# Performance work log

Measured on AMD Instinct MI355X. Metric: run time of the kernel, lower is better.

## Reference

```python
import jax, jax.numpy as jnp
import numpy as np

N = 100000      # number of entities
E = 400000      # number of edges (before self-loops)
D = 200         # feature_dim
D0 = 100        # init_fea_dim
NREL = 475      # 2*num_rels + 1 (self-loop relation = NREL-1)
NBR = 100       # num_base_r
B = 1024        # query batch
L = 2           # number of cells / layers
EPS = 1e-5


def _bn(x, g, b):
    # BatchNorm1d, training-mode batch statistics (biased var), per-feature affine
    m = jnp.mean(x, axis=0)
    v = jnp.var(x, axis=0)
    return (x - m) * jax.lax.rsqrt(v + EPS) * g + b


def setup_inputs() -> dict:
    key = jax.random.key(0)
    ks = jax.random.split(key, 12)
    return {
        # graph (edge list form of the DGL graph g)
        "src_id": jax.random.randint(ks[0], (E,), 0, N),
        "dst_id": jax.random.randint(ks[1], (E,), 0, N),
        "e_type": jax.random.randint(ks[2], (E,), 0, NREL - 1),  # NREL-1 reserved for self-loop
        # link-prediction queries
        "subj": jax.random.randint(ks[3], (B,), 0, N),
        "rel": jax.random.randint(ks[4], (B,), 0, NREL),
        # learned parameters
        "emb_h": jax.random.normal(ks[5], (N, D0), dtype=jnp.float32) * 0.02,
        "emb_e": jax.random.normal(ks[6], (NBR, D), dtype=jnp.float32) * 0.1,
        "lin_w": jax.random.normal(ks[7], (D0, D), dtype=jnp.float32) * (1.0 / np.sqrt(D0)),
        "lin_b": jnp.zeros((D,), dtype=jnp.float32),
        "rel_wt": jax.random.normal(ks[8], (NREL, NBR), dtype=jnp.float32) * 0.1,
        "w_rel": jax.random.normal(ks[9], (D, D), dtype=jnp.float32) * (1.0 / np.sqrt(D)),
        # per-cell params, stacked over L layers
        "agg_bn_g": jnp.ones((L, D), dtype=jnp.float32),
        "agg_bn_b": jnp.zeros((L, D), dtype=jnp.float32),
        "cell_bn_g": jnp.ones((L, D), dtype=jnp.float32),
        "cell_bn_b": jnp.zeros((L, D), dtype=jnp.float32),
        "concat_w": jax.random.normal(ks[10], (L, D, D), dtype=jnp.float32) * (1.0 / np.sqrt(D)),
        "concat_b": jnp.zeros((L, D), dtype=jnp.float32),
    }


def reference(src_id, dst_id, e_type, subj, rel,
              emb_h, emb_e, lin_w, lin_b, rel_wt, w_rel,
              agg_bn_g, agg_bn_b, cell_bn_g, cell_bn_b, concat_w, concat_b):
    nodes = jnp.arange(N, dtype=src_id.dtype)
    # append self-loops for every node, with the dedicated self-loop relation id
    src_f = jnp.concatenate([src_id, nodes])                      # [E+N]
    dst_f = jnp.concatenate([dst_id, nodes])                      # [E+N]
    et_f = jnp.concatenate([e_type, jnp.full((N,), NREL - 1, dtype=e_type.dtype)])

    all_ent = emb_h @ lin_w + lin_b                               # [N, D]
    rel_embed = rel_wt @ emb_e                                    # [NREL, D]

    for i in range(L):
        src_emb = all_ent[src_f]                                  # [E+N, D] per-edge gather
        hr = rel_embed[et_f]                                      # [E+N, D] per-edge gather
        zero_out = src_emb * hr                                   # pre_mult op (no BN/ReLU)
        agg = jax.ops.segment_sum(zero_out, dst_f, num_segments=N)  # edge -> node aggregation
        agg = jax.nn.relu(_bn(agg, agg_bn_g[i], agg_bn_b[i]))     # OpModule BN + ReLU
        h = agg @ concat_w[i] + concat_b[i]                       # Cell concat Linear (1 concat node)
        all_ent = jax.nn.relu(_bn(h, cell_bn_g[i], cell_bn_b[i]))  # Cell BN + ReLU
        rel_embed = rel_embed @ w_rel                             # per-layer relation transform

    # DistMult score function: [B, N]
    score = (all_ent[subj] * rel_embed[rel]) @ all_ent.T
    return score
```

## Files before the change

### kernel.cpp

```cpp
#include <hip/hip_runtime.h>


#define N_ENT  100000
#define N_EDGE 400000
#define N_EF   500000
#define D_     200
#define D0_    100
#define NREL_  475
#define B_     1024
#define GSTAT2 2048
#define KP_D   224
#define KP_D0  128

typedef unsigned short ushort_t;
typedef __attribute__((ext_vector_type(8))) short bf16x8;
typedef __attribute__((ext_vector_type(4))) float f32x4;

__device__ __forceinline__ ushort_t f2bf(float x) {
  unsigned u = __float_as_uint(x);
  return (ushort_t)((u + 0x7FFFu + ((u >> 16) & 1u)) >> 16);
}
__device__ __forceinline__ float bf2f(ushort_t h) {
  return __uint_as_float(((unsigned)h) << 16);
}

__device__ __forceinline__ void gld16(const void* g, void* l) {
  __builtin_amdgcn_global_load_lds(
      (const __attribute__((address_space(1))) unsigned*)g,
      (__attribute__((address_space(3))) unsigned*)l, 16, 0, 0);
}


__global__ void k_hist(const int* __restrict__ dst_id, int* __restrict__ cnt) {
  int e = blockIdx.x * 256 + threadIdx.x;
  if (e < N_EF) {
    int d = (e < N_EDGE) ? dst_id[e] : (e - N_EDGE);
    atomicAdd(&cnt[d], 1);
  }
}

__global__ __launch_bounds__(256) void k_scan_block(const int* __restrict__ cnt,
                                                    int* __restrict__ rp,
                                                    int* __restrict__ bsum) {
  __shared__ int sm[256];
  int tid = threadIdx.x;
  int base = blockIdx.x * 1024 + tid * 4;
  int v0 = (base + 0 < N_ENT) ? cnt[base + 0] : 0;
  int v1 = (base + 1 < N_ENT) ? cnt[base + 1] : 0;
  int v2 = (base + 2 < N_ENT) ? cnt[base + 2] : 0;
  int v3 = (base + 3 < N_ENT) ? cnt[base + 3] : 0;
  int tsum = v0 + v1 + v2 + v3;
  sm[tid] = tsum;
  __syncthreads();
  for (int off = 1; off < 256; off <<= 1) {
    int t = (tid >= off) ? sm[tid - off] : 0;
    __syncthreads();
    sm[tid] += t;
    __syncthreads();
  }
  int run = sm[tid] - tsum;
  if (base + 0 < N_ENT) { rp[base + 0] = run; } run += v0;
  if (base + 1 < N_ENT) { rp[base + 1] = run; } run += v1;
  if (base + 2 < N_ENT) { rp[base + 2] = run; } run += v2;
  if (base + 3 < N_ENT) { rp[base + 3] = run; }
  if (tid == 255) bsum[blockIdx.x] = sm[255];
}

__global__ void k_scan_tops(int* __restrict__ bsum, int nb) {
  __shared__ int sm[256];
  int tid = threadIdx.x;
  int v = (tid < nb) ? bsum[tid] : 0;
  sm[tid] = v;
  __syncthreads();
  for (int off = 1; off < 256; off <<= 1) {
    int t = (tid >= off) ? sm[tid - off] : 0;
    __syncthreads();
    sm[tid] += t;
    __syncthreads();
  }
  if (tid < nb) bsum[tid] = sm[tid] - v;
}

__global__ void k_scan_add(int* __restrict__ rp, const int* __restrict__ bsum,
                           int* __restrict__ cursor) {
  int i = blockIdx.x * 256 + threadIdx.x;
  if (i < N_ENT) {
    int r = rp[i] + bsum[i >> 10];
    rp[i] = r;
    cursor[i] = r;
  }
}

__global__ void k_fill(const int* __restrict__ src_id, const int* __restrict__ dst_id,
                       const int* __restrict__ e_type, int* __restrict__ cursor,
                       int* __restrict__ cs, int* __restrict__ ct) {
  int e = blockIdx.x * 256 + threadIdx.x;
  if (e < N_EF) {
    int s, d, t;
    if (e < N_EDGE) { s = src_id[e]; d = dst_id[e]; t = e_type[e]; }
    else            { s = e - N_EDGE; d = s; t = NREL_ - 1; }
    int pos = atomicAdd(&cursor[d], 1);
    cs[pos] = s;
    ct[pos] = t;
  }
}


template <bool BN>
__global__ __launch_bounds__(256) void k_aggregate(const float* __restrict__ ent,
                                                   const float* __restrict__ relE,
                                                   const int* __restrict__ rp,
                                                   const int* __restrict__ cnt,
                                                   const int* __restrict__ cs,
                                                   const int* __restrict__ ct,
                                                   float* __restrict__ out,
                                                   const float* __restrict__ scale,
                                                   const float* __restrict__ shift) {
  int n = blockIdx.x;
  int f = threadIdx.x;
  if (f >= D_) return;
  float sc = 0.f, sh = 0.f;
  if (BN) { sc = scale[f]; sh = shift[f]; }
  int s0 = rp[n], e0 = s0 + cnt[n];
  float a0 = 0.f, a1 = 0.f, a2 = 0.f, a3 = 0.f;
  int idx = s0;
  for (; idx + 4 <= e0; idx += 4) {
    int sA = cs[idx + 0], tA = ct[idx + 0];
    int sB = cs[idx + 1], tB = ct[idx + 1];
    int sC = cs[idx + 2], tC = ct[idx + 2];
    int sD = cs[idx + 3], tD = ct[idx + 3];
    float eA = ent[(long)sA * D_ + f], rA = relE[(long)tA * D_ + f];
    float eB = ent[(long)sB * D_ + f], rB = relE[(long)tB * D_ + f];
    float eC = ent[(long)sC * D_ + f], rC = relE[(long)tC * D_ + f];
    float eD = ent[(long)sD * D_ + f], rD = relE[(long)tD * D_ + f];
    if (BN) {
      eA = fmaxf(fmaf(eA, sc, sh), 0.f);
      eB = fmaxf(fmaf(eB, sc, sh), 0.f);
      eC = fmaxf(fmaf(eC, sc, sh), 0.f);
      eD = fmaxf(fmaf(eD, sc, sh), 0.f);
    }
    a0 = fmaf(eA, rA, a0);
    a1 = fmaf(eB, rB, a1);
    a2 = fmaf(eC, rC, a2);
    a3 = fmaf(eD, rD, a3);
  }
  for (; idx < e0; ++idx) {
    int sA = cs[idx], tA = ct[idx];
    float eA = ent[(long)sA * D_ + f];
    if (BN) eA = fmaxf(fmaf(eA, sc, sh), 0.f);
    a0 = fmaf(eA, relE[(long)tA * D_ + f], a0);
  }
  out[(long)n * D_ + f] = (a0 + a1) + (a2 + a3);
}

__global__ __launch_bounds__(64) void k_colstats(const float* __restrict__ X,
                                                 double* __restrict__ part) {
  int t = threadIdx.x;
  if (t >= 50) return;
  double s0 = 0, s1 = 0, s2 = 0, s3 = 0, q0 = 0, q1 = 0, q2 = 0, q3 = 0;
  for (int r = blockIdx.x; r < N_ENT; r += GSTAT2) {
    float4 v = *(const float4*)(X + (long)r * D_ + t * 4);
    s0 += v.x; q0 += (double)v.x * v.x;
    s1 += v.y; q1 += (double)v.y * v.y;
    s2 += v.z; q2 += (double)v.z * v.z;
    s3 += v.w; q3 += (double)v.w * v.w;
  }
  long o = (long)blockIdx.x * 400 + t * 4;
  part[o + 0] = s0; part[o + 1] = s1; part[o + 2] = s2; part[o + 3] = s3;
  part[o + 200] = q0; part[o + 201] = q1; part[o + 202] = q2; part[o + 203] = q3;
}

__global__ __launch_bounds__(256) void k_bn_fin(const double* __restrict__ part,
                                                const float* __restrict__ g,
                                                const float* __restrict__ b,
                                                float* __restrict__ scale,
                                                float* __restrict__ shift) {
  int f = blockIdx.x;
  int tid = threadIdx.x;
  double S = 0.0, S2 = 0.0;
  for (int i = tid; i < GSTAT2; i += 256) {
    S += part[(long)i * 400 + f];
    S2 += part[(long)i * 400 + 200 + f];
  }
  __shared__ double smS[256], smS2[256];
  smS[tid] = S; smS2[tid] = S2;
  __syncthreads();
  for (int off = 128; off > 0; off >>= 1) {
    if (tid < off) { smS[tid] += smS[tid + off]; smS2[tid] += smS2[tid + off]; }
    __syncthreads();
  }
  if (tid == 0) {
    double mean = smS[0] / N_ENT;
    double var = smS2[0] / N_ENT - mean * mean;
    double inv = 1.0 / sqrt(var + 1e-5);
    float sc = g[f] * (float)inv;
    scale[f] = sc;
    shift[f] = b[f] - (float)mean * sc;
  }
}

__global__ void k_norm_split(float* __restrict__ X, const float* __restrict__ scale,
                             const float* __restrict__ shift,
                             ushort_t* __restrict__ H, ushort_t* __restrict__ L) {
  const long total = (long)N_ENT * (KP_D / 4);
  for (long i4 = (long)blockIdx.x * 256 + threadIdx.x; i4 < total;
       i4 += (long)gridDim.x * 256) {
    int r = (int)(i4 / (KP_D / 4));
    int c4 = (int)(i4 % (KP_D / 4)) * 4;
    float vv[4] = {0.f, 0.f, 0.f, 0.f};
    if (c4 < D_) {
      float4 v = *(float4*)(X + (long)r * D_ + c4);
      vv[0] = fmaxf(fmaf(v.x, scale[c4 + 0], shift[c4 + 0]), 0.f);
      vv[1] = fmaxf(fmaf(v.y, scale[c4 + 1], shift[c4 + 1]), 0.f);
      vv[2] = fmaxf(fmaf(v.z, scale[c4 + 2], shift[c4 + 2]), 0.f);
      vv[3] = fmaxf(fmaf(v.w, scale[c4 + 3], shift[c4 + 3]), 0.f);
      *(float4*)(X + (long)r * D_ + c4) = make_float4(vv[0], vv[1], vv[2], vv[3]);
    }
    ushort_t h[4], l[4];
#pragma unroll
    for (int t = 0; t < 4; t++) {
      h[t] = f2bf(vv[t]);
      l[t] = f2bf(vv[t] - bf2f(h[t]));
    }
    long o = (long)r * KP_D + c4;
    *(uint2*)(H + o) = make_uint2((unsigned)h[0] | ((unsigned)h[1] << 16),
                                  (unsigned)h[2] | ((unsigned)h[3] << 16));
    *(uint2*)(L + o) = make_uint2((unsigned)l[0] | ((unsigned)l[1] << 16),
                                  (unsigned)l[2] | ((unsigned)l[3] << 16));
  }
}

__global__ void k_tsplit(const float* __restrict__ W, int K, int Nc, int Kp,
                         ushort_t* __restrict__ H, ushort_t* __restrict__ L) {
  int i = blockIdx.x * 256 + threadIdx.x;
  if (i >= Nc * Kp) return;
  int n = i / Kp, kp = i - n * Kp;
  float v = (kp < K) ? W[(long)kp * Nc + n] : 0.f;
  ushort_t h = f2bf(v);
  H[i] = h;
  L[i] = f2bf(v - bf2f(h));
}

__global__ void k_qsplit(const float* __restrict__ ent, const float* __restrict__ relE,
                         const int* __restrict__ subj, const int* __restrict__ rel,
                         ushort_t* __restrict__ H, ushort_t* __restrict__ L) {
  int i = blockIdx.x * 256 + threadIdx.x;
  if (i >= B_ * KP_D) return;
  int b = i / KP_D, kp = i - b * KP_D;
  float v = 0.f;
  if (kp < D_)
    v = ent[(long)subj[b] * D_ + kp] * relE[(long)rel[b] * D_ + kp];
  ushort_t h = f2bf(v);
  H[i] = h;
  L[i] = f2bf(v - bf2f(h));
}

template <bool SWZ>
__global__ __launch_bounds__(256, 2) void k_mfma_pre(
    const ushort_t* __restrict__ Ah, const ushort_t* __restrict__ Al,
    const ushort_t* __restrict__ Bh, const ushort_t* __restrict__ Bl,
    float* __restrict__ C, int M, int Nc, int Kp, long ldc) {
  __shared__ __align__(16) ushort_t lds[2 * 16384];
  const int tid = threadIdx.x;
  const int wave = tid >> 6, lane = tid & 63;
  int bxi, byi;
  if (SWZ) {
    int orig = blockIdx.x;
    int cpx = gridDim.x >> 3;
    int swz = (orig & 7) * cpx + (orig >> 3);
    bxi = swz & 7;
    byi = swz >> 3;
  } else {
    bxi = blockIdx.x;
    byi = blockIdx.y;
  }
  const int bm = bxi * 128, bn = byi * 128;
  const int wr = (wave >> 1) * 64, wc = (wave & 1) * 64;
  const int l15 = lane & 15, l4 = lane >> 4;
  const int NT = Kp >> 5;

  f32x4 acc[4][4] = {};

  auto stage = [&](int kt, int ph) {
#pragma unroll
    for (int j = 0; j < 8; ++j) {
      int c = wave * 8 + j;
      int buf = c >> 3;
      int r = (c & 7) * 16 + (lane >> 2);
      int sg = (lane & 3) ^ ((r >> 1) & 3);
      const ushort_t* bp;
      int rowg;
      if (buf == 0)      { bp = Ah; rowg = bm + r; if (rowg > M - 1) rowg = M - 1; }
      else if (buf == 1) { bp = Al; rowg = bm + r; if (rowg > M - 1) rowg = M - 1; }
      else if (buf == 2) { bp = Bh; rowg = bn + r; if (rowg > Nc - 1) rowg = Nc - 1; }
      else               { bp = Bl; rowg = bn + r; if (rowg > Nc - 1) rowg = Nc - 1; }
      gld16(bp + (long)rowg * Kp + kt * 32 + sg * 8, lds + ph * 16384 + c * 512);
    }
  };

  stage(0, 0);
  __syncthreads();
  int p = 0;
  for (int t = 0; t < NT; ++t) {
    if (t + 1 < NT) stage(t + 1, p ^ 1);
    const ushort_t* base = lds + p * 16384;
    bf16x8 a_h[4], a_l[4], b_h[4], b_l[4];
#pragma unroll
    for (int i = 0; i < 4; i++) {
      int rA = wr + i * 16 + l15;
      int sA = (l4 ^ ((rA >> 1) & 3)) * 8;
      a_h[i] = *(const bf16x8*)(base + rA * 32 + sA);
      a_l[i] = *(const bf16x8*)(base + 4096 + rA * 32 + sA);
      int rB = wc + i * 16 + l15;
      int sB = (l4 ^ ((rB >> 1) & 3)) * 8;
      b_h[i] = *(const bf16x8*)(base + 8192 + rB * 32 + sB);
      b_l[i] = *(const bf16x8*)(base + 12288 + rB * 32 + sB);
    }
#pragma unroll
    for (int i = 0; i < 4; i++)
#pragma unroll
      for (int j = 0; j < 4; j++) {
        acc[i][j] = __builtin_amdgcn_mfma_f32_16x16x32_bf16(a_h[i], b_h[j], acc[i][j], 0, 0, 0);
        acc[i][j] = __builtin_amdgcn_mfma_f32_16x16x32_bf16(a_l[i], b_h[j], acc[i][j], 0, 0, 0);
        acc[i][j] = __builtin_amdgcn_mfma_f32_16x16x32_bf16(a_h[i], b_l[j], acc[i][j], 0, 0, 0);
      }
    __syncthreads();
    p ^= 1;
  }

#pragma unroll
  for (int i = 0; i < 4; i++) {
    int mrow = bm + wr + i * 16 + l4 * 4;
#pragma unroll
    for (int j = 0; j < 4; j++) {
      int n = bn + wc + j * 16 + l15;
      if (n >= Nc) continue;
#pragma unroll
      for (int v = 0; v < 4; v++) {
        int m = mrow + v;
        if (m < M) C[(long)m * ldc + n] = acc[i][j][v];
      }
    }
  }
}

template <bool BN_A, bool HAS_BIAS>
__global__ __launch_bounds__(256, 2) void k_mfma_af32(
    const float* __restrict__ A, int lda, int K,
    const ushort_t* __restrict__ Bh, const ushort_t* __restrict__ Bl,
    float* __restrict__ C, int M, int Nc, int Kp, long ldc,
    const float* __restrict__ scale, const float* __restrict__ shift,
    const float* __restrict__ bias) {
  __shared__ __align__(16) ushort_t lds[2 * 16384];
  __shared__ float sc_lds[KP_D], sh_lds[KP_D];
  const int tid = threadIdx.x;
  const int wave = tid >> 6, lane = tid & 63;
  const int bm = blockIdx.x * 128, bn = blockIdx.y * 128;
  const int wr = (wave >> 1) * 64, wc = (wave & 1) * 64;
  const int l15 = lane & 15, l4 = lane >> 4;
  const int NT = Kp >> 5;

  if (BN_A) {
    for (int i = tid; i < Kp; i += 256) {
      sc_lds[i] = (i < K) ? scale[i] : 0.f;
      sh_lds[i] = (i < K) ? shift[i] : 0.f;
    }
    __syncthreads();
  }

  const int ar = tid >> 1;
  const int acb = (tid & 1) * 16;
  int arow = bm + ar; if (arow > M - 1) arow = M - 1;
  const int aswz = (ar >> 1) & 3;
  const int s0 = (((acb >> 3) + 0) ^ aswz) * 8;
  const int s1 = (((acb >> 3) + 1) ^ aswz) * 8;

  auto loadA = [&](int kt, float4* va) {
    int kc = kt * 32 + acb;
    const float* ap = A + (long)arow * lda + kc;
    if (kc + 16 <= K) {
#pragma unroll
      for (int q = 0; q < 4; q++) va[q] = *(const float4*)(ap + q * 4);
    } else {
#pragma unroll
      for (int q = 0; q < 4; q++) {
        float t0 = (kc + q * 4 + 0 < K) ? ap[q * 4 + 0] : 0.f;
        float t1 = (kc + q * 4 + 1 < K) ? ap[q * 4 + 1] : 0.f;
        float t2 = (kc + q * 4 + 2 < K) ? ap[q * 4 + 2] : 0.f;
        float t3 = (kc + q * 4 + 3 < K) ? ap[q * 4 + 3] : 0.f;
        va[q] = make_float4(t0, t1, t2, t3);
      }
    }
  };

  auto writeA = [&](int kt, int ph, float4* va) {
    float v[16];
#pragma unroll
    for (int q = 0; q < 4; q++) {
      v[q * 4 + 0] = va[q].x; v[q * 4 + 1] = va[q].y;
      v[q * 4 + 2] = va[q].z; v[q * 4 + 3] = va[q].w;
    }
    if (BN_A) {
      int kc = kt * 32 + acb;
#pragma unroll
      for (int e = 0; e < 16; e++) {
        int col = kc + e;
        if (col < K) v[e] = fmaxf(fmaf(v[e], sc_lds[col], sh_lds[col]), 0.f);
      }
    }
    unsigned hh[8], ll[8];
#pragma unroll
    for (int e = 0; e < 8; e++) {
      ushort_t h0 = f2bf(v[2 * e]), h1 = f2bf(v[2 * e + 1]);
      ushort_t l0 = f2bf(v[2 * e] - bf2f(h0)), l1 = f2bf(v[2 * e + 1] - bf2f(h1));
      hh[e] = (unsigned)h0 | ((unsigned)h1 << 16);
      ll[e] = (unsigned)l0 | ((unsigned)l1 << 16);
    }
    ushort_t* baseA = lds + ph * 16384 + ar * 32;
    *(uint4*)(baseA + s0) = make_uint4(hh[0], hh[1], hh[2], hh[3]);
    *(uint4*)(baseA + s1) = make_uint4(hh[4], hh[5], hh[6], hh[7]);
    ushort_t* baseL = baseA + 4096;
    *(uint4*)(baseL + s0) = make_uint4(ll[0], ll[1], ll[2], ll[3]);
    *(uint4*)(baseL + s1) = make_uint4(ll[4], ll[5], ll[6], ll[7]);
  };

  auto stageB = [&](int kt, int ph) {
#pragma unroll
    for (int j = 0; j < 4; ++j) {
      int c = 16 + wave * 4 + j;
      int buf = c >> 3;
      int r = (c & 7) * 16 + (lane >> 2);
      int sg = (lane & 3) ^ ((r >> 1) & 3);
      const ushort_t* bp = (buf == 2) ? Bh : Bl;
      int rowg = bn + r; if (rowg > Nc - 1) rowg = Nc - 1;
      gld16(bp + (long)rowg * Kp + kt * 32 + sg * 8, lds + ph * 16384 + c * 512);
    }
  };

  f32x4 acc[4][4] = {};
  {
    float4 va[4];
    loadA(0, va);
    writeA(0, 0, va);
    stageB(0, 0);
  }
  __syncthreads();
  int p = 0;
  for (int t = 0; t < NT; ++t) {
    float4 va[4];
    const bool pre = (t + 1 < NT);
    if (pre) {
      loadA(t + 1, va);
      stageB(t + 1, p ^ 1);
    }
    const ushort_t* base = lds + p * 16384;
    bf16x8 a_h[4], a_l[4], b_h[4], b_l[4];
#pragma unroll
    for (int i = 0; i < 4; i++) {
      int rA = wr + i * 16 + l15;
      int sA = (l4 ^ ((rA >> 1) & 3)) * 8;
      a_h[i] = *(const bf16x8*)(base + rA * 32 + sA);
      a_l[i] = *(const bf16x8*)(base + 4096 + rA * 32 + sA);
      int rB = wc + i * 16 + l15;
      int sB = (l4 ^ ((rB >> 1) & 3)) * 8;
      b_h[i] = *(const bf16x8*)(base + 8192 + rB * 32 + sB);
      b_l[i] = *(const bf16x8*)(base + 12288 + rB * 32 + sB);
    }
#pragma unroll
    for (int i = 0; i < 4; i++)
#pragma unroll
      for (int j = 0; j < 4; j++) {
        acc[i][j] = __builtin_amdgcn_mfma_f32_16x16x32_bf16(a_h[i], b_h[j], acc[i][j], 0, 0, 0);
        acc[i][j] = __builtin_amdgcn_mfma_f32_16x16x32_bf16(a_l[i], b_h[j], acc[i][j], 0, 0, 0);
        acc[i][j] = __builtin_amdgcn_mfma_f32_16x16x32_bf16(a_h[i], b_l[j], acc[i][j], 0, 0, 0);
      }
    if (pre) writeA(t + 1, p ^ 1, va);
    __syncthreads();
    p ^= 1;
  }

#pragma unroll
  for (int i = 0; i < 4; i++) {
    int mrow = bm + wr + i * 16 + l4 * 4;
#pragma unroll
    for (int j = 0; j < 4; j++) {
      int n = bn + wc + j * 16 + l15;
      if (n >= Nc) continue;
      float bb = HAS_BIAS ? bias[n] : 0.f;
#pragma unroll
      for (int v = 0; v < 4; v++) {
        int m = mrow + v;
        if (m < M) C[(long)m * ldc + n] = acc[i][j][v] + bb;
      }
    }
  }
}

template <int TM, int TN>
__global__ __launch_bounds__(256) void k_gemm_abt(
    const float* __restrict__ A, const float* __restrict__ Bm, float* __restrict__ C,
    int M, int Nc, int K, long ldc) {
  constexpr int BM = TM * 16, BN = TN * 16, KC = 20;
  __shared__ float As[BM * KC];
  __shared__ float Bs[BN * KC];
  const int tid = threadIdx.x;
  const int tx = tid & 15, ty = tid >> 4;
  const int bm = blockIdx.x * BM, bn = blockIdx.y * BN;
  float acc[TM][TN];
#pragma unroll
  for (int i = 0; i < TM; i++)
#pragma unroll
    for (int j = 0; j < TN; j++) acc[i][j] = 0.f;
  for (int kc = 0; kc < K; kc += KC) {
    for (int i4 = tid; i4 < BM * 5; i4 += 256) {
      int r = i4 / 5, kq = (i4 - r * 5) * 4;
      int row = bm + r; if (row > M - 1) row = M - 1;
      *(float4*)(As + r * KC + kq) = *(const float4*)(A + (long)row * K + kc + kq);
    }
    for (int i4 = tid; i4 < BN * 5; i4 += 256) {
      int r = i4 / 5, kq = (i4 - r * 5) * 4;
      int row = bn + r; if (row > Nc - 1) row = Nc - 1;
      *(float4*)(Bs + r * KC + kq) = *(const float4*)(Bm + (long)row * K + kc + kq);
    }
    __syncthreads();
#pragma unroll
    for (int k4 = 0; k4 < KC; k4 += 4) {
      float4 af[TM], bf[TN];
#pragma unroll
      for (int i = 0; i < TM; i++) af[i] = *(const float4*)(As + (i * 16 + ty) * KC + k4);
#pragma unroll
      for (int j = 0; j < TN; j++) bf[j] = *(const float4*)(Bs + (j * 16 + tx) * KC + k4);
#pragma unroll
      for (int i = 0; i < TM; i++)
#pragma unroll
        for (int j = 0; j < TN; j++) {
          acc[i][j] = fmaf(af[i].x, bf[j].x, acc[i][j]);
          acc[i][j] = fmaf(af[i].y, bf[j].y, acc[i][j]);
          acc[i][j] = fmaf(af[i].z, bf[j].z, acc[i][j]);
          acc[i][j] = fmaf(af[i].w, bf[j].w, acc[i][j]);
        }
    }
    __syncthreads();
  }
#pragma unroll
  for (int i = 0; i < TM; i++) {
    int m = bm + i * 16 + ty;
    if (m >= M) continue;
#pragma unroll
    for (int j = 0; j < TN; j++) {
      int n = bn + j * 16 + tx;
      if (n < Nc) C[(long)m * ldc + n] = acc[i][j];
    }
  }
}

__global__ void k_transpose(const float* __restrict__ s, float* __restrict__ d, int R, int C) {
  int i = blockIdx.x * 256 + threadIdx.x;
  if (i < R * C) { int r = i / C, c = i - r * C; d[c * R + r] = s[i]; }
}


extern "C" void kernel_launch(void* const* d_in, const int* in_sizes, int n_in,
                              void* d_out, int out_size, void* d_ws, size_t ws_size,
                              hipStream_t stream) {
  const int* src_id = (const int*)d_in[0];
  const int* dst_id = (const int*)d_in[1];
  const int* e_type = (const int*)d_in[2];
  const int* subj = (const int*)d_in[3];
  const int* rel = (const int*)d_in[4];
  const float* emb_h = (const float*)d_in[5];
  const float* emb_e = (const float*)d_in[6];
  const float* lin_w = (const float*)d_in[7];
  const float* lin_b = (const float*)d_in[8];
  const float* rel_wt = (const float*)d_in[9];
  const float* w_rel = (const float*)d_in[10];
  const float* agg_bn_g = (const float*)d_in[11];
  const float* agg_bn_b = (const float*)d_in[12];
  const float* cell_bn_g = (const float*)d_in[13];
  const float* cell_bn_b = (const float*)d_in[14];
  const float* concat_w = (const float*)d_in[15];
  const float* concat_b = (const float*)d_in[16];
  float* out = (float*)d_out;

  char* w = (char*)d_ws;
  ushort_t* ent_h = (ushort_t*)(w + 0);
  ushort_t* ent_l = (ushort_t*)(w + 44800000);
  ushort_t* q_h   = (ushort_t*)(w + 89600000);
  ushort_t* q_l   = (ushort_t*)(w + 90112000);

  char* ob = (char*)d_out;
  float* ent    = (float*)(ob + 0);
  float* tmp    = (float*)(ob + 80000000);
  double* part  = (double*)(ob + 160000000);
  int* counts   = (int*)(ob + 166600000);
  int* row_ptr  = (int*)(ob + 167000000);
  int* cursor   = (int*)(ob + 167400000);
  int* csr_src  = (int*)(ob + 167800000);
  int* csr_et   = (int*)(ob + 169800000);
  float* relA   = (float*)(ob + 171800000);
  float* relB   = (float*)(ob + 172180000);
  float* embeT  = (float*)(ob + 172560000);
  float* wrT    = (float*)(ob + 172640000);
  ushort_t* linw_h = (ushort_t*)(ob + 172800000);
  ushort_t* linw_l = (ushort_t*)(ob + 172851200);
  ushort_t* cw0_h  = (ushort_t*)(ob + 172902400);
  ushort_t* cw0_l  = (ushort_t*)(ob + 172992000);
  ushort_t* cw1_h  = (ushort_t*)(ob + 173081600);
  ushort_t* cw1_l  = (ushort_t*)(ob + 173171200);
  float* scaleb = (float*)(ob + 173260800);
  float* shiftb = (float*)(ob + 173261824);
  int* bsum     = (int*)(ob + 173262848);

  hipMemsetAsync(counts, 0, N_ENT * sizeof(int), stream);
  k_hist<<<(N_EF + 255) / 256, 256, 0, stream>>>(dst_id, counts);
  const int NB = (N_ENT + 1023) / 1024;
  k_scan_block<<<NB, 256, 0, stream>>>(counts, row_ptr, bsum);
  k_scan_tops<<<1, 256, 0, stream>>>(bsum, NB);
  k_scan_add<<<(N_ENT + 255) / 256, 256, 0, stream>>>(row_ptr, bsum, cursor);
  k_fill<<<(N_EF + 255) / 256, 256, 0, stream>>>(src_id, dst_id, e_type, cursor,
                                                 csr_src, csr_et);

  k_tsplit<<<(D_ * KP_D0 + 255) / 256, 256, 0, stream>>>(lin_w, D0_, D_, KP_D0,
                                                         linw_h, linw_l);
  k_tsplit<<<(D_ * KP_D + 255) / 256, 256, 0, stream>>>(concat_w, D_, D_, KP_D,
                                                        cw0_h, cw0_l);
  k_tsplit<<<(D_ * KP_D + 255) / 256, 256, 0, stream>>>(concat_w + D_ * D_, D_, D_,
                                                        KP_D, cw1_h, cw1_l);
  k_transpose<<<(D0_ * D_ + 255) / 256, 256, 0, stream>>>(emb_e, embeT, D0_, D_);
  k_transpose<<<(D_ * D_ + 255) / 256, 256, 0, stream>>>(w_rel, wrT, D_, D_);

  const int GM = (N_ENT + 127) / 128;

  k_mfma_af32<false, true><<<dim3(GM, 2), 256, 0, stream>>>(
      emb_h, D0_, D0_, linw_h, linw_l, ent, N_ENT, D_, KP_D0, (long)D_,
      nullptr, nullptr, lin_b);
  k_gemm_abt<8, 4><<<dim3(4, 4), 256, 0, stream>>>(rel_wt, embeT, relA, NREL_, D_,
                                                   D0_, (long)D_);

  k_aggregate<false><<<N_ENT, 256, 0, stream>>>(ent, relA, row_ptr, counts,
                                                csr_src, csr_et, tmp, nullptr, nullptr);
  k_colstats<<<GSTAT2, 64, 0, stream>>>(tmp, part);
  k_bn_fin<<<D_, 256, 0, stream>>>(part, agg_bn_g, agg_bn_b, scaleb, shiftb);
  k_mfma_af32<true, true><<<dim3(GM, 2), 256, 0, stream>>>(
      tmp, D_, D_, cw0_h, cw0_l, ent, N_ENT, D_, KP_D, (long)D_,
      scaleb, shiftb, concat_b);
  k_colstats<<<GSTAT2, 64, 0, stream>>>(ent, part);
  k_bn_fin<<<D_, 256, 0, stream>>>(part, cell_bn_g, cell_bn_b, scaleb, shiftb);
  k_gemm_abt<8, 4><<<dim3(4, 4), 256, 0, stream>>>(relA, wrT, relB, NREL_, D_, D_,
                                                   (long)D_);

  k_aggregate<true><<<N_ENT, 256, 0, stream>>>(ent, relB, row_ptr, counts,
                                               csr_src, csr_et, tmp, scaleb, shiftb);
  k_colstats<<<GSTAT2, 64, 0, stream>>>(tmp, part);
  k_bn_fin<<<D_, 256, 0, stream>>>(part, agg_bn_g + D_, agg_bn_b + D_, scaleb, shiftb);
  k_mfma_af32<true, true><<<dim3(GM, 2), 256, 0, stream>>>(
      tmp, D_, D_, cw1_h, cw1_l, ent, N_ENT, D_, KP_D, (long)D_,
      scaleb, shiftb, concat_b + D_);
  k_colstats<<<GSTAT2, 64, 0, stream>>>(ent, part);
  k_bn_fin<<<D_, 256, 0, stream>>>(part, cell_bn_g + D_, cell_bn_b + D_, scaleb, shiftb);
  k_norm_split<<<2048, 256, 0, stream>>>(ent, scaleb, shiftb, ent_h, ent_l);
  k_gemm_abt<8, 4><<<dim3(4, 4), 256, 0, stream>>>(relB, wrT, relA, NREL_, D_, D_,
                                                   (long)D_);

  k_qsplit<<<(B_ * KP_D + 255) / 256, 256, 0, stream>>>(ent, relA, subj, rel,
                                                        q_h, q_l);

  k_mfma_pre<true><<<dim3((B_ / 128) * GM), 256, 0, stream>>>(
      q_h, q_l, ent_h, ent_l, out, B_, N_ENT, KP_D, (long)N_ENT);
}
```

Measured before the change: 1.129 ms.

## Handle self-loops inside aggregation and retile score GEMM to 64x128 blocks

Self-loop edges are no longer put into the CSR. Each aggregation block now adds its own node's self-loop term directly, which cuts the histogram and fill atomics and the CSR size by N entries. The final score GEMM drops from 128x128 to 64x128 tiles with a compile-time K loop that is fully unrolled. This doubles the block count and lowers register and LDS use, in exchange for more B-tile reloads from global memory.

```diff
diff --git a/kernel.cpp b/kernel.cpp
--- a/kernel.cpp
+++ b/kernel.cpp
@@ -3,7 +3,6 @@
 
 #define N_ENT  100000
 #define N_EDGE 400000
-#define N_EF   500000
 #define D_     200
 #define D0_    100
 #define NREL_  475
@@ -33,10 +32,7 @@
 
 __global__ void k_hist(const int* __restrict__ dst_id, int* __restrict__ cnt) {
   int e = blockIdx.x * 256 + threadIdx.x;
-  if (e < N_EF) {
-    int d = (e < N_EDGE) ? dst_id[e] : (e - N_EDGE);
-    atomicAdd(&cnt[d], 1);
-  }
+  if (e < N_EDGE) atomicAdd(&cnt[dst_id[e]], 1);
 }
 
 __global__ __launch_bounds__(256) void k_scan_block(const int* __restrict__ cnt,
@@ -95,13 +91,10 @@
                        const int* __restrict__ e_type, int* __restrict__ cursor,
                        int* __restrict__ cs, int* __restrict__ ct) {
   int e = blockIdx.x * 256 + threadIdx.x;
-  if (e < N_EF) {
-    int s, d, t;
-    if (e < N_EDGE) { s = src_id[e]; d = dst_id[e]; t = e_type[e]; }
-    else            { s = e - N_EDGE; d = s; t = NREL_ - 1; }
-    int pos = atomicAdd(&cursor[d], 1);
-    cs[pos] = s;
-    ct[pos] = t;
+  if (e < N_EDGE) {
+    int pos = atomicAdd(&cursor[dst_id[e]], 1);
+    cs[pos] = src_id[e];
+    ct[pos] = e_type[e];
   }
 }
 
@@ -121,8 +114,11 @@
   if (f >= D_) return;
   float sc = 0.f, sh = 0.f;
   if (BN) { sc = scale[f]; sh = shift[f]; }
+  float selfE = ent[(long)n * D_ + f];
+  if (BN) selfE = fmaxf(fmaf(selfE, sc, sh), 0.f);
+  float a0 = selfE * relE[(long)(NREL_ - 1) * D_ + f];
+  float a1 = 0.f, a2 = 0.f, a3 = 0.f;
   int s0 = rp[n], e0 = s0 + cnt[n];
-  float a0 = 0.f, a1 = 0.f, a2 = 0.f, a3 = 0.f;
   int idx = s0;
   for (; idx + 4 <= e0; idx += 4) {
     int sA = cs[idx + 0], tA = ct[idx + 0];
@@ -256,11 +252,13 @@
 }
 
 template <bool SWZ>
-__global__ __launch_bounds__(256, 2) void k_mfma_pre(
+__global__ __launch_bounds__(256, 2) void k_score(
     const ushort_t* __restrict__ Ah, const ushort_t* __restrict__ Al,
     const ushort_t* __restrict__ Bh, const ushort_t* __restrict__ Bl,
-    float* __restrict__ C, int M, int Nc, int Kp, long ldc) {
-  __shared__ __align__(16) ushort_t lds[2 * 16384];
+    float* __restrict__ C, int M, int Nc, long ldc) {
+  constexpr int KP = KP_D;
+  constexpr int NT = KP / 32;
+  __shared__ __align__(16) ushort_t lds[2 * 12288];
   const int tid = threadIdx.x;
   const int wave = tid >> 6, lane = tid & 63;
   int bxi, byi;
@@ -268,56 +266,58 @@
     int orig = blockIdx.x;
     int cpx = gridDim.x >> 3;
     int swz = (orig & 7) * cpx + (orig >> 3);
-    bxi = swz & 7;
-    byi = swz >> 3;
+    bxi = swz & 15;
+    byi = swz >> 4;
   } else {
     bxi = blockIdx.x;
     byi = blockIdx.y;
   }
-  const int bm = bxi * 128, bn = byi * 128;
-  const int wr = (wave >> 1) * 64, wc = (wave & 1) * 64;
+  const int bm = bxi * 64, bn = byi * 128;
+  const int wr = (wave >> 1) * 32, wc = (wave & 1) * 64;
   const int l15 = lane & 15, l4 = lane >> 4;
-  const int NT = Kp >> 5;
-
-  f32x4 acc[4][4] = {};
+
+  f32x4 acc[2][4] = {};
 
   auto stage = [&](int kt, int ph) {
 #pragma unroll
-    for (int j = 0; j < 8; ++j) {
-      int c = wave * 8 + j;
-      int buf = c >> 3;
-      int r = (c & 7) * 16 + (lane >> 2);
-      int sg = (lane & 3) ^ ((r >> 1) & 3);
+    for (int j = 0; j < 6; ++j) {
+      int c = wave * 6 + j;
+      int r;
       const ushort_t* bp;
       int rowg;
-      if (buf == 0)      { bp = Ah; rowg = bm + r; if (rowg > M - 1) rowg = M - 1; }
-      else if (buf == 1) { bp = Al; rowg = bm + r; if (rowg > M - 1) rowg = M - 1; }
-      else if (buf == 2) { bp = Bh; rowg = bn + r; if (rowg > Nc - 1) rowg = Nc - 1; }
-      else               { bp = Bl; rowg = bn + r; if (rowg > Nc - 1) rowg = Nc - 1; }
-      gld16(bp + (long)rowg * Kp + kt * 32 + sg * 8, lds + ph * 16384 + c * 512);
+      if (c < 4)       { r = c * 16 + (lane >> 2);        bp = Ah; rowg = bm + r; }
+      else if (c < 8)  { r = (c - 4) * 16 + (lane >> 2);  bp = Al; rowg = bm + r; }
+      else if (c < 16) { r = (c - 8) * 16 + (lane >> 2);  bp = Bh; rowg = bn + r; if (rowg > Nc - 1) rowg = Nc - 1; }
+      else             { r = (c - 16) * 16 + (lane >> 2); bp = Bl; rowg = bn + r; if (rowg > Nc - 1) rowg = Nc - 1; }
+      int sg = (lane & 3) ^ ((r >> 1) & 3);
+      gld16(bp + (long)rowg * KP + kt * 32 + sg * 8, lds + ph * 12288 + c * 512);
     }
   };
 
   stage(0, 0);
   __syncthreads();
   int p = 0;
+#pragma unroll
   for (int t = 0; t < NT; ++t) {
     if (t + 1 < NT) stage(t + 1, p ^ 1);
-    const ushort_t* base = lds + p * 16384;
-    bf16x8 a_h[4], a_l[4], b_h[4], b_l[4];
-#pragma unroll
-    for (int i = 0; i < 4; i++) {
+    const ushort_t* base = lds + p * 12288;
+    bf16x8 a_h[2], a_l[2], b_h[4], b_l[4];
+#pragma unroll
+    for (int i = 0; i < 2; i++) {
       int rA = wr + i * 16 + l15;
-      int sA = (l4 ^ ((rA >> 1) & 3)) * 8;
-      a_h[i] = *(const bf16x8*)(base + rA * 32 + sA);
-      a_l[i] = *(const bf16x8*)(base + 4096 + rA * 32 + sA);
-      int rB = wc + i * 16 + l15;
-      int sB = (l4 ^ ((rB >> 1) & 3)) * 8;
-      b_h[i] = *(const bf16x8*)(base + 8192 + rB * 32 + sB);
-      b_l[i] = *(const bf16x8*)(base + 12288 + rB * 32 + sB);
-    }
-#pragma unroll
-    for (int i = 0; i < 4; i++)
+      int s = (l4 ^ ((rA >> 1) & 3)) * 8;
+      a_h[i] = *(const bf16x8*)(base + rA * 32 + s);
+      a_l[i] = *(const bf16x8*)(base + 2048 + rA * 32 + s);
+    }
+#pragma unroll
+    for (int j = 0; j < 4; j++) {
+      int rB = wc + j * 16 + l15;
+      int s = (l4 ^ ((rB >> 1) & 3)) * 8;
+      b_h[j] = *(const bf16x8*)(base + 4096 + rB * 32 + s);
+      b_l[j] = *(const bf16x8*)(base + 8192 + rB * 32 + s);
+    }
+#pragma unroll
+    for (int i = 0; i < 2; i++)
 #pragma unroll
       for (int j = 0; j < 4; j++) {
         acc[i][j] = __builtin_amdgcn_mfma_f32_16x16x32_bf16(a_h[i], b_h[j], acc[i][j], 0, 0, 0);
@@ -329,7 +329,7 @@
   }
 
 #pragma unroll
-  for (int i = 0; i < 4; i++) {
+  for (int i = 0; i < 2; i++) {
     int mrow = bm + wr + i * 16 + l4 * 4;
 #pragma unroll
     for (int j = 0; j < 4; j++) {
@@ -596,7 +596,7 @@
   int* row_ptr  = (int*)(ob + 167000000);
   int* cursor   = (int*)(ob + 167400000);
   int* csr_src  = (int*)(ob + 167800000);
-  int* csr_et   = (int*)(ob + 169800000);
+  int* csr_et   = (int*)(ob + 169400000);
   float* relA   = (float*)(ob + 171800000);
   float* relB   = (float*)(ob + 172180000);
   float* embeT  = (float*)(ob + 172560000);
@@ -612,13 +612,13 @@
   int* bsum     = (int*)(ob + 173262848);
 
   hipMemsetAsync(counts, 0, N_ENT * sizeof(int), stream);
-  k_hist<<<(N_EF + 255) / 256, 256, 0, stream>>>(dst_id, counts);
+  k_hist<<<(N_EDGE + 255) / 256, 256, 0, stream>>>(dst_id, counts);
   const int NB = (N_ENT + 1023) / 1024;
   k_scan_block<<<NB, 256, 0, stream>>>(counts, row_ptr, bsum);
   k_scan_tops<<<1, 256, 0, stream>>>(bsum, NB);
   k_scan_add<<<(N_ENT + 255) / 256, 256, 0, stream>>>(row_ptr, bsum, cursor);
-  k_fill<<<(N_EF + 255) / 256, 256, 0, stream>>>(src_id, dst_id, e_type, cursor,
-                                                 csr_src, csr_et);
+  k_fill<<<(N_EDGE + 255) / 256, 256, 0, stream>>>(src_id, dst_id, e_type, cursor,
+                                                   csr_src, csr_et);
 
   k_tsplit<<<(D_ * KP_D0 + 255) / 256, 256, 0, stream>>>(lin_w, D0_, D_, KP_D0,
                                                          linw_h, linw_l);
@@ -665,6 +665,6 @@
   k_qsplit<<<(B_ * KP_D + 255) / 256, 256, 0, stream>>>(ent, relA, subj, rel,
                                                         q_h, q_l);
 
-  k_mfma_pre<true><<<dim3((B_ / 128) * GM), 256, 0, stream>>>(
-      q_h, q_l, ent_h, ent_l, out, B_, N_ENT, KP_D, (long)N_ENT);
-}
+  k_score<true><<<dim3((B_ / 64) * GM), 256, 0, stream>>>(
+      q_h, q_l, ent_h, ent_l, out, B_, N_ENT, (long)N_ENT);
+}
```

Result: no change. 1.131 ms (+0.2%).
